# Kernel tuning notes

Measured on AMD Instinct MI355X. Metric: run time of the kernel, lower is better.

The kernel has to match this reference:

```python
import jax, jax.numpy as jnp
import numpy as np

B, N, IDIM, ODIM = 4096, 32, 1024, 1024


def setup_inputs() -> dict:
    key = jax.random.key(0)
    k1, k2, k3 = jax.random.split(key, 3)
    x = jax.random.normal(k1, (B, IDIM), dtype=jnp.float32)
    weight = jax.random.normal(k2, (N, ODIM, IDIM), dtype=jnp.float32)
    gate_w = jax.random.normal(k3, (N, IDIM), dtype=jnp.float32) * (1.0 / np.sqrt(IDIM))
    gate_b = jnp.zeros((N,), dtype=jnp.float32)
    return {"x": x, "weight": weight, "gate_w": gate_w, "gate_b": gate_b}


def reference(x, weight, gate_w, gate_b):
    # per-expert projection: [b, n, odim] (the large intermediate the torch code
    # materializes via einsum 'noi,biz->bnoz' with z=1)
    y = jnp.einsum('noi,bi->bno', weight, x)
    # gate weights: gelu(Linear(idim -> n)) ; torch gelu default is exact (erf)
    g = jax.nn.gelu(x @ gate_w.T + gate_b, approximate=False)  # [b, n]
    # gated combine over experts (the `y @ g` step after rearrange)
    out = jnp.einsum('bno,bn->bo', y, g)  # [b, odim]
    return out
```

## Files before the change

kernel.cpp:

```cpp
#include <hip/hip_runtime.h>
#include <hip/hip_bf16.h>
#include <math.h>


#define BSZ  4096
#define NEXP 32
#define IDIM 1024
#define ODIM 1024

typedef __attribute__((ext_vector_type(8))) short bf16x8;
typedef __attribute__((ext_vector_type(4))) float f32x4;

#define GLOAD_LDS16(g, l) __builtin_amdgcn_global_load_lds( \
    (const __attribute__((address_space(1))) void*)(g),     \
    (__attribute__((address_space(3))) void*)(l), 16, 0, 0)

__device__ __forceinline__ unsigned short f2bf(float f) {
  unsigned u = __float_as_uint(f);
  unsigned r = (u + 0x7FFFu + ((u >> 16) & 1u)) >> 16;
  return (unsigned short)r;
}

__global__ void zero_kernel(float* __restrict__ out) {
  int i = blockIdx.x * blockDim.x + threadIdx.x;
  ((float4*)out)[i] = make_float4(0.f, 0.f, 0.f, 0.f);
}

__global__ void conv_kernel(const float* __restrict__ in, unsigned short* __restrict__ outb) {
  int i = blockIdx.x * blockDim.x + threadIdx.x;
  const float4* p = (const float4*)in + (size_t)i * 2;
  float4 a = p[0], b = p[1];
  union { bf16x8 v; unsigned short s[8]; } o;
  o.s[0] = f2bf(a.x); o.s[1] = f2bf(a.y); o.s[2] = f2bf(a.z); o.s[3] = f2bf(a.w);
  o.s[4] = f2bf(b.x); o.s[5] = f2bf(b.y); o.s[6] = f2bf(b.z); o.s[7] = f2bf(b.w);
  ((bf16x8*)outb)[i] = o.v;
}

__global__ void gate_kernel(const float* __restrict__ x, const float* __restrict__ gw,
                            const float* __restrict__ gb, float* __restrict__ gT) {
  const int lane = threadIdx.x & 63;
  const int row = blockIdx.x * 4 + (threadIdx.x >> 6);
  const float4* xr = (const float4*)(x + (size_t)row * IDIM);
  float4 xv[4];
#pragma unroll
  for (int t = 0; t < 4; ++t) xv[t] = xr[t * 64 + lane];
  for (int n = 0; n < NEXP; ++n) {
    const float4* wr = (const float4*)(gw + (size_t)n * IDIM);
    float s = 0.f;
#pragma unroll
    for (int t = 0; t < 4; ++t) {
      float4 wv = wr[t * 64 + lane];
      s += xv[t].x * wv.x + xv[t].y * wv.y + xv[t].z * wv.z + xv[t].w * wv.w;
    }
#pragma unroll
    for (int off = 32; off > 0; off >>= 1) s += __shfl_down(s, off, 64);
    if (lane == 0) {
      float v = s + gb[n];
      gT[(size_t)n * BSZ + row] = 0.5f * v * (1.0f + erff(v * 0.70710678118f));
    }
  }
}

__global__ __launch_bounds__(256, 2) void gemm_kernel(
    const unsigned short* __restrict__ xb,
    const unsigned short* __restrict__ wb,
    const float* __restrict__ gT,
    float* __restrict__ out)
{
  __shared__ unsigned short As[2][128 * 64];
  __shared__ unsigned short Bs[2][128 * 64];

  const int tid  = threadIdx.x;
  const int lane = tid & 63;
  const int wid  = tid >> 6;
  const int wm   = wid >> 1, wn = wid & 1;

  const int orig  = blockIdx.x;
  const int wgid  = (orig & 7) * 128 + (orig >> 3);
  const int mtile = wgid & 31;
  const int group = wgid >> 5;
  const int split = group & 3;
  const int col0  = (group >> 2) * 128;
  const int row0  = mtile * 128;

  const int srow = lane >> 3;
  const int jsrc = (lane & 7) ^ srow;
  size_t a_off[4], b_off[4];
#pragma unroll
  for (int c4 = 0; c4 < 4; ++c4) {
    const int c = wid * 4 + c4;
    a_off[c4] = (size_t)(row0 + c * 8 + srow) * IDIM + jsrc * 8;
    b_off[c4] = (size_t)(col0 + c * 8 + srow) * IDIM + jsrc * 8;
  }

  const int frow = lane & 15;
  const int hi   = lane >> 4;

  f32x4 acc[4][4], acc_e[4][4];
#pragma unroll
  for (int i = 0; i < 4; ++i)
#pragma unroll
    for (int j = 0; j < 4; ++j) {
      acc[i][j]   = f32x4{0.f, 0.f, 0.f, 0.f};
      acc_e[i][j] = f32x4{0.f, 0.f, 0.f, 0.f};
    }

  auto STAGE = [&](int buf, int kt) {
    const int n  = kt >> 4;
    const int i0 = (kt & 15) << 6;
    const unsigned short* wb_n = wb + ((size_t)(split * 8 + n) << 20);
#pragma unroll
    for (int c4 = 0; c4 < 4; ++c4) {
      GLOAD_LDS16(xb + a_off[c4] + i0,   &As[buf][(wid * 4 + c4) * 512]);
      GLOAD_LDS16(wb_n + b_off[c4] + i0, &Bs[buf][(wid * 4 + c4) * 512]);
    }
  };

  STAGE(0, 0);
  __syncthreads();

  int cur = 0;
  for (int kt = 0; kt < 128; ++kt) {
    if (kt < 127) STAGE(cur ^ 1, kt + 1);

    bf16x8 af[4][2], bfr[4][2];
#pragma unroll
    for (int mi = 0; mi < 4; ++mi)
#pragma unroll
      for (int kk = 0; kk < 2; ++kk) {
        const int r = wm * 64 + mi * 16 + frow;
        const int g = ((kk << 2) + hi) ^ (frow & 7);
        af[mi][kk] = *(const bf16x8*)&As[cur][r * 64 + g * 8];
      }
#pragma unroll
    for (int ni = 0; ni < 4; ++ni)
#pragma unroll
      for (int kk = 0; kk < 2; ++kk) {
        const int r = wn * 64 + ni * 16 + frow;
        const int g = ((kk << 2) + hi) ^ (frow & 7);
        bfr[ni][kk] = *(const bf16x8*)&Bs[cur][r * 64 + g * 8];
      }
#pragma unroll
    for (int mi = 0; mi < 4; ++mi)
#pragma unroll
      for (int ni = 0; ni < 4; ++ni)
#pragma unroll
        for (int kk = 0; kk < 2; ++kk)
          acc_e[mi][ni] = __builtin_amdgcn_mfma_f32_16x16x32_bf16(
              af[mi][kk], bfr[ni][kk], acc_e[mi][ni], 0, 0, 0);

    if ((kt & 15) == 15) {
      const int n = kt >> 4;
      const float* gp = gT + ((size_t)(split * 8 + n) << 12) + row0 + wm * 64 + hi * 4;
#pragma unroll
      for (int mi = 0; mi < 4; ++mi) {
        float4 gv = *(const float4*)(gp + mi * 16);
        f32x4 g4 = f32x4{gv.x, gv.y, gv.z, gv.w};
#pragma unroll
        for (int ni = 0; ni < 4; ++ni) {
          acc[mi][ni] += g4 * acc_e[mi][ni];
          acc_e[mi][ni] = f32x4{0.f, 0.f, 0.f, 0.f};
        }
      }
    }

    __syncthreads();
    cur ^= 1;
  }

  const int orow0 = row0 + wm * 64 + hi * 4;
  const int ocol0 = col0 + wn * 64 + frow;
#pragma unroll
  for (int mi = 0; mi < 4; ++mi)
#pragma unroll
    for (int j = 0; j < 4; ++j) {
      const int r = orow0 + mi * 16 + j;
#pragma unroll
      for (int ni = 0; ni < 4; ++ni)
        atomicAdd(out + (size_t)r * ODIM + ocol0 + ni * 16, acc[mi][ni][j]);
    }
}

extern "C" void kernel_launch(void* const* d_in, const int* in_sizes, int n_in,
                              void* d_out, int out_size, void* d_ws, size_t ws_size,
                              hipStream_t stream) {
  const float* x  = (const float*)d_in[0];
  const float* w  = (const float*)d_in[1];
  const float* gw = (const float*)d_in[2];
  const float* gb = (const float*)d_in[3];
  float* out = (float*)d_out;

  unsigned short* xb   = (unsigned short*)d_ws;
  unsigned short* wbuf = (unsigned short*)((char*)d_ws + (8u << 20));
  float*          gT   = (float*)((char*)d_ws + (72u << 20));

  zero_kernel<<<(BSZ * ODIM / 4) / 256, 256, 0, stream>>>(out);
  conv_kernel<<<(BSZ * IDIM / 8) / 256, 256, 0, stream>>>(x, xb);
  conv_kernel<<<(NEXP * ODIM * IDIM / 8) / 256, 256, 0, stream>>>(w, wbuf);
  gate_kernel<<<BSZ / 4, 256, 0, stream>>>(x, gw, gb, gT);

  gemm_kernel<<<1024, 256, 0, stream>>>(xb, wbuf, gT, out);
}
```

Before: 373.0 us.

## Enlarge GEMM tile to 256x128 with 512 threads and triple-buffered pipeline

The gated-expert GEMM now uses 512-thread blocks covering 256 rows by 128 columns, with experts split in two instead of four, so each block runs 16 experts. That halves the number of output atomics and reuses each B tile across more rows. A triple-buffered LDS ring with explicit vmcnt waits and a single barrier per k-step replaces the double buffer with two syncs. The gate values are preloaded into LDS, and MFMA issue is split into two halves with raised priority. The larger LDS footprint and the 256-block grid may lower occupancy and leave some CUs idle.

Result: slower. 419.7 us (+12.5%).

```diff
diff --git a/kernel.cpp b/kernel.cpp
--- a/kernel.cpp
+++ b/kernel.cpp
@@ -14,6 +14,13 @@
 #define GLOAD_LDS16(g, l) __builtin_amdgcn_global_load_lds( \
     (const __attribute__((address_space(1))) void*)(g),     \
     (__attribute__((address_space(3))) void*)(l), 16, 0, 0)
+
+#define WAITV6 asm volatile("s_waitcnt vmcnt(6)" ::: "memory")
+#define WAITV0 asm volatile("s_waitcnt vmcnt(0)" ::: "memory")
+#define WAITL0 do { asm volatile("s_waitcnt lgkmcnt(0)" ::: "memory"); \
+                    __builtin_amdgcn_sched_barrier(0); } while (0)
+#define BARRIER do { __builtin_amdgcn_s_barrier(); \
+                     __builtin_amdgcn_sched_barrier(0); } while (0)
 
 __device__ __forceinline__ unsigned short f2bf(float f) {
   unsigned u = __float_as_uint(f);
@@ -61,37 +68,39 @@
   }
 }
 
-__global__ __launch_bounds__(256, 2) void gemm_kernel(
+__global__ __launch_bounds__(512, 2) void gemm_kernel(
     const unsigned short* __restrict__ xb,
     const unsigned short* __restrict__ wb,
     const float* __restrict__ gT,
     float* __restrict__ out)
 {
-  __shared__ unsigned short As[2][128 * 64];
-  __shared__ unsigned short Bs[2][128 * 64];
+  __shared__ unsigned short As[3][256 * 64];
+  __shared__ unsigned short Bs[3][128 * 64];
+  __shared__ float g_lds[16][256];
 
   const int tid  = threadIdx.x;
   const int lane = tid & 63;
   const int wid  = tid >> 6;
-  const int wm   = wid >> 1, wn = wid & 1;
+  const int wm   = wid >> 1;
+  const int wn   = wid & 1;
 
   const int orig  = blockIdx.x;
-  const int wgid  = (orig & 7) * 128 + (orig >> 3);
-  const int mtile = wgid & 31;
-  const int group = wgid >> 5;
-  const int split = group & 3;
-  const int col0  = (group >> 2) * 128;
-  const int row0  = mtile * 128;
+  const int wgid  = (orig & 7) * 32 + (orig >> 3);
+  const int mtile = wgid & 15;
+  const int grp   = wgid >> 4;
+  const int split = grp & 1;
+  const int col0  = (grp >> 1) * 128;
+  const int row0  = mtile * 256;
 
   const int srow = lane >> 3;
   const int jsrc = (lane & 7) ^ srow;
-  size_t a_off[4], b_off[4];
-#pragma unroll
-  for (int c4 = 0; c4 < 4; ++c4) {
-    const int c = wid * 4 + c4;
-    a_off[c4] = (size_t)(row0 + c * 8 + srow) * IDIM + jsrc * 8;
-    b_off[c4] = (size_t)(col0 + c * 8 + srow) * IDIM + jsrc * 8;
-  }
+  size_t a_off[4], b_off[2];
+#pragma unroll
+  for (int l = 0; l < 4; ++l)
+    a_off[l] = (size_t)(row0 + (wid * 4 + l) * 8 + srow) * IDIM + jsrc * 8;
+#pragma unroll
+  for (int l = 0; l < 2; ++l)
+    b_off[l] = (size_t)(col0 + (wid * 2 + l) * 8 + srow) * IDIM + jsrc * 8;
 
   const int frow = lane & 15;
   const int hi   = lane >> 4;
@@ -105,56 +114,95 @@
       acc_e[i][j] = f32x4{0.f, 0.f, 0.f, 0.f};
     }
 
+  {
+    const int e = tid >> 5;
+    const int r = (tid & 31) * 8;
+    const float* src = gT + ((size_t)(split * 16 + e) << 12) + row0 + r;
+    *(float4*)&g_lds[e][r]     = *(const float4*)src;
+    *(float4*)&g_lds[e][r + 4] = *(const float4*)(src + 4);
+  }
+
   auto STAGE = [&](int buf, int kt) {
-    const int n  = kt >> 4;
+    const int e  = kt >> 4;
     const int i0 = (kt & 15) << 6;
-    const unsigned short* wb_n = wb + ((size_t)(split * 8 + n) << 20);
-#pragma unroll
-    for (int c4 = 0; c4 < 4; ++c4) {
-      GLOAD_LDS16(xb + a_off[c4] + i0,   &As[buf][(wid * 4 + c4) * 512]);
-      GLOAD_LDS16(wb_n + b_off[c4] + i0, &Bs[buf][(wid * 4 + c4) * 512]);
-    }
+    const unsigned short* wb_n = wb + ((size_t)(split * 16 + e) << 20);
+#pragma unroll
+    for (int l = 0; l < 4; ++l)
+      GLOAD_LDS16(xb + a_off[l] + i0, &As[buf][(wid * 4 + l) * 512]);
+#pragma unroll
+    for (int l = 0; l < 2; ++l)
+      GLOAD_LDS16(wb_n + b_off[l] + i0, &Bs[buf][(wid * 2 + l) * 512]);
   };
 
+  __syncthreads();
   STAGE(0, 0);
-  __syncthreads();
+  STAGE(1, 1);
 
   int cur = 0;
-  for (int kt = 0; kt < 128; ++kt) {
-    if (kt < 127) STAGE(cur ^ 1, kt + 1);
-
-    bf16x8 af[4][2], bfr[4][2];
-#pragma unroll
-    for (int mi = 0; mi < 4; ++mi)
+#pragma unroll 1
+  for (int kt = 0; kt < 256; ++kt) {
+    if (kt == 255) { WAITV0; } else { WAITV6; }
+    BARRIER;
+    if (kt < 254) { int s = cur + 2; if (s >= 3) s -= 3; STAGE(s, kt + 2); }
+
+    const unsigned short* A_ = &As[cur][0];
+    const unsigned short* B_ = &Bs[cur][0];
+
+    bf16x8 bfr[4][2], afA[2][2];
+#pragma unroll
+    for (int ni = 0; ni < 4; ++ni)
+#pragma unroll
+      for (int kk = 0; kk < 2; ++kk) {
+        const int r = wn * 64 + ni * 16 + frow;
+        const int g = ((kk << 2) + hi) ^ (frow & 7);
+        bfr[ni][kk] = *(const bf16x8*)&B_[r * 64 + g * 8];
+      }
+#pragma unroll
+    for (int mi = 0; mi < 2; ++mi)
 #pragma unroll
       for (int kk = 0; kk < 2; ++kk) {
         const int r = wm * 64 + mi * 16 + frow;
         const int g = ((kk << 2) + hi) ^ (frow & 7);
-        af[mi][kk] = *(const bf16x8*)&As[cur][r * 64 + g * 8];
-      }
-#pragma unroll
-    for (int ni = 0; ni < 4; ++ni)
-#pragma unroll
-      for (int kk = 0; kk < 2; ++kk) {
-        const int r = wn * 64 + ni * 16 + frow;
-        const int g = ((kk << 2) + hi) ^ (frow & 7);
-        bfr[ni][kk] = *(const bf16x8*)&Bs[cur][r * 64 + g * 8];
-      }
-#pragma unroll
-    for (int mi = 0; mi < 4; ++mi)
+        afA[mi][kk] = *(const bf16x8*)&A_[r * 64 + g * 8];
+      }
+    WAITL0;
+    __builtin_amdgcn_s_setprio(1);
+#pragma unroll
+    for (int mi = 0; mi < 2; ++mi)
 #pragma unroll
       for (int ni = 0; ni < 4; ++ni)
 #pragma unroll
         for (int kk = 0; kk < 2; ++kk)
           acc_e[mi][ni] = __builtin_amdgcn_mfma_f32_16x16x32_bf16(
-              af[mi][kk], bfr[ni][kk], acc_e[mi][ni], 0, 0, 0);
+              afA[mi][kk], bfr[ni][kk], acc_e[mi][ni], 0, 0, 0);
+    __builtin_amdgcn_s_setprio(0);
+
+    bf16x8 afB[2][2];
+#pragma unroll
+    for (int mi = 0; mi < 2; ++mi)
+#pragma unroll
+      for (int kk = 0; kk < 2; ++kk) {
+        const int r = wm * 64 + (mi + 2) * 16 + frow;
+        const int g = ((kk << 2) + hi) ^ (frow & 7);
+        afB[mi][kk] = *(const bf16x8*)&A_[r * 64 + g * 8];
+      }
+    WAITL0;
+    __builtin_amdgcn_s_setprio(1);
+#pragma unroll
+    for (int mi = 0; mi < 2; ++mi)
+#pragma unroll
+      for (int ni = 0; ni < 4; ++ni)
+#pragma unroll
+        for (int kk = 0; kk < 2; ++kk)
+          acc_e[mi + 2][ni] = __builtin_amdgcn_mfma_f32_16x16x32_bf16(
+              afB[mi][kk], bfr[ni][kk], acc_e[mi + 2][ni], 0, 0, 0);
+    __builtin_amdgcn_s_setprio(0);
 
     if ((kt & 15) == 15) {
-      const int n = kt >> 4;
-      const float* gp = gT + ((size_t)(split * 8 + n) << 12) + row0 + wm * 64 + hi * 4;
+      const int e = kt >> 4;
 #pragma unroll
       for (int mi = 0; mi < 4; ++mi) {
-        float4 gv = *(const float4*)(gp + mi * 16);
+        float4 gv = *(const float4*)&g_lds[e][wm * 64 + mi * 16 + hi * 4];
         f32x4 g4 = f32x4{gv.x, gv.y, gv.z, gv.w};
 #pragma unroll
         for (int ni = 0; ni < 4; ++ni) {
@@ -163,9 +211,7 @@
         }
       }
     }
-
-    __syncthreads();
-    cur ^= 1;
+    if (++cur == 3) cur = 0;
   }
 
   const int orow0 = row0 + wm * 64 + hi * 4;
@@ -199,5 +245,5 @@
   conv_kernel<<<(NEXP * ODIM * IDIM / 8) / 256, 256, 0, stream>>>(w, wbuf);
   gate_kernel<<<BSZ / 4, 256, 0, stream>>>(x, gw, gb, gT);
 
-  gemm_kernel<<<1024, 256, 0, stream>>>(xb, wbuf, gT, out);
-}
+  gemm_kernel<<<256, 512, 0, stream>>>(xb, wbuf, gT, out);
+}
```
